# Performance work log

Hardware: AMD Instinct MI355X
Metric: run time of the kernel (lower is better)

Reference implementation:

```python
import jax, jax.numpy as jnp
import numpy as np

B, C, H, W = 4, 64, 128, 128
KS = 3
PAD = 1
N = KS * KS


def conv2d(x, w, b=None, stride=1, padding=0):
    out = jax.lax.conv_general_dilated(
        x, w, (stride, stride), [(padding, padding), (padding, padding)],
        dimension_numbers=("NCHW", "OIHW", "NCHW"))
    if b is not None:
        out = out + b[None, :, None, None]
    return out


def setup_inputs() -> dict:
    key = jax.random.key(0)
    ks = jax.random.split(key, 6)
    scale = 0.05  # small weights so offsets stay in a realistic range
    return {
        "x": jax.random.normal(ks[0], (B, C, H, W), jnp.float32),
        "p_w": jax.random.normal(ks[1], (2 * N, C, 3, 3), jnp.float32) * scale,
        "p_b": jax.random.normal(ks[2], (2 * N,), jnp.float32) * scale,
        "m_w": jax.random.normal(ks[3], (N, C, 3, 3), jnp.float32) * scale,
        "m_b": jax.random.normal(ks[4], (N,), jnp.float32) * scale,
        "conv_w": jax.random.normal(ks[5], (C, C, KS, KS), jnp.float32) * (1.0 / np.sqrt(C * N)),
    }


def reference(x, p_w, p_b, m_w, m_b, conv_w):
    b, c, h, w = x.shape
    # offset / modulation branches (stride=1, padding=1, 3x3)
    offset = conv2d(x, p_w, p_b, 1, 1)                 # (b, 2N, h, w)
    m = jax.nn.sigmoid(conv2d(x, m_w, m_b, 1, 1))      # (b, N,  h, w)

    xp = jnp.pad(x, ((0, 0), (0, 0), (PAD, PAD), (PAD, PAD)))
    Hp, Wp = h + 2 * PAD, w + 2 * PAD

    # sampling positions p = p_0 + p_n + offset, layout (b, h, w, 2N): first N rows(x), last N cols(y)
    pnx, pny = jnp.meshgrid(jnp.arange(-1, 2), jnp.arange(-1, 2), indexing="ij")
    p_n = jnp.concatenate([pnx.ravel(), pny.ravel()]).astype(x.dtype)          # (2N,)
    base_x = jnp.broadcast_to(jnp.arange(1, h + 1)[:, None, None], (h, w, N))
    base_y = jnp.broadcast_to(jnp.arange(1, w + 1)[None, :, None], (h, w, N))
    base = jnp.concatenate([base_x, base_y], axis=-1).astype(x.dtype)          # (h, w, 2N)
    p = jnp.transpose(offset, (0, 2, 3, 1)) + p_n + base[None]                 # (b, h, w, 2N)

    px, py = p[..., :N], p[..., N:]
    # integer corners from detached p (floor), clamped to padded extent
    qf = jnp.floor(jax.lax.stop_gradient(p))
    qx_lt = jnp.clip(qf[..., :N], 0, Hp - 1).astype(jnp.int32)
    qy_lt = jnp.clip(qf[..., N:], 0, Wp - 1).astype(jnp.int32)
    qx_rb = jnp.clip(qf[..., :N] + 1, 0, Hp - 1).astype(jnp.int32)
    qy_rb = jnp.clip(qf[..., N:] + 1, 0, Wp - 1).astype(jnp.int32)

    pxc = jnp.clip(px, 0, Hp - 1)
    pyc = jnp.clip(py, 0, Wp - 1)

    g_lt = (1 + (qx_lt - pxc)) * (1 + (qy_lt - pyc))
    g_rb = (1 - (qx_rb - pxc)) * (1 - (qy_rb - pyc))
    g_lb = (1 + (qx_lt - pxc)) * (1 - (qy_rb - pyc))
    g_rt = (1 - (qx_rb - pxc)) * (1 + (qy_lt - pyc))

    xp_flat = xp.reshape(b, c, Hp * Wp)

    def gather(qx, qy):
        idx = (qx * Wp + qy).reshape(b, -1)                     # (b, h*w*N)
        out = jax.vmap(lambda xf, i: xf[:, i])(xp_flat, idx)    # (b, c, h*w*N)
        return out.reshape(b, c, h, w, N)

    x_off = (g_lt[:, None] * gather(qx_lt, qy_lt)
             + g_rb[:, None] * gather(qx_rb, qy_rb)
             + g_lb[:, None] * gather(qx_lt, qy_rb)
             + g_rt[:, None] * gather(qx_rb, qy_lt))            # (b, c, h, w, N)

    x_off = x_off * jnp.transpose(m, (0, 2, 3, 1))[:, None]     # modulation

    # _reshape_x_offset: n = 3*i + j -> (b, c, h*3, w*3) with layout (h, i, w, j)
    x_off = x_off.reshape(b, c, h, w, KS, KS)
    x_off = jnp.transpose(x_off, (0, 1, 2, 4, 3, 5)).reshape(b, c, h * KS, w * KS)

    return conv2d(x_off, conv_w, None, stride=KS, padding=0)    # (b, outc, h, w)
```

## Files before the change

### kernel.cpp

```cpp
#include <hip/hip_runtime.h>
#include <hip/hip_bf16.h>
#include <math.h>

#define BB 4
#define CC 64
#define HH 128
#define WW 128
#define NPT 9
#define HW (HH*WW)
#define HP 130
#define WP 130

typedef __attribute__((ext_vector_type(8))) short bf16x8;
typedef __attribute__((ext_vector_type(4))) float f32x4;

static __device__ __forceinline__ unsigned short f2bf(float f) {
    __hip_bfloat16 h = __float2bfloat16(f);
    return *reinterpret_cast<unsigned short*>(&h);
}
static __device__ __forceinline__ float bf2f(unsigned short u) {
    return __uint_as_float(((unsigned int)u) << 16);
}

__global__ void k_prep(const float* __restrict__ cw,
                       const float* __restrict__ pw, const float* __restrict__ pb,
                       const float* __restrict__ mw, const float* __restrict__ mb,
                       unsigned short* __restrict__ wtt, unsigned short* __restrict__ wttB,
                       float* __restrict__ b27, unsigned short* __restrict__ xt) {
    int i = blockIdx.x * 256 + threadIdx.x;
    if (i < 36864) {
        int cot = i / 9216;
        int rem = i - cot * 9216;
        int n   = rem >> 10;
        int s2  = (rem >> 9) & 1;
        int lhi = (rem >> 7) & 3;
        int l15 = (rem >> 3) & 15;
        int j   = i & 7;
        int co = cot * 16 + l15;
        int ci = s2 * 32 + lhi * 8 + j;
        wtt[i] = f2bf(cw[(co * 64 + ci) * 9 + n]);
    } else if (i < 55296) {
        int q = i - 36864;
        int j   = q & 7;
        int co  = (q >> 3) & 31;
        int lhi = (q >> 8) & 3;
        int s2  = (q >> 10) & 1;
        int n   = q >> 11;
        int ci  = s2 * 32 + lhi * 8 + j;
        float v = 0.f;
        if (co < 18) v = pw[(co * 64 + ci) * 9 + n];
        else if (co < 27) v = mw[((co - 18) * 64 + ci) * 9 + n];
        wttB[q] = f2bf(v);
    } else if (i < 55328) {
        int co = i - 55296;
        b27[co] = (co < 18) ? pb[co] : (co < 27 ? mb[co - 18] : 0.f);
    } else if (i < 55328 + BB * 4128) {
        int p = i - 55328;
        int b = p / 4128, r = p - b * 4128;
        size_t base;
        if (r < 2080) {
            int row = r / 1040;
            int rr  = r - row * 1040;
            int wp = rr >> 3, c8 = rr & 7;
            int hp = row ? (HP - 1) : 0;
            base = (((size_t)b * HP + hp) * WP + wp) * 64 + c8 * 8;
        } else {
            int r2 = r - 2080;
            int col = r2 >> 10;
            int rr  = r2 & 1023;
            int hp = (rr >> 3) + 1, c8 = rr & 7;
            int wp = col ? (WP - 1) : 0;
            base = (((size_t)b * HP + hp) * WP + wp) * 64 + c8 * 8;
        }
        *reinterpret_cast<int4*>(xt + base) = make_int4(0, 0, 0, 0);
    }
}

__global__ __launch_bounds__(256) void k_nhwc(const float* __restrict__ x,
                                              unsigned short* __restrict__ xt) {
    __shared__ float tile[64][129];
    int blk = blockIdx.x;
    int b = blk >> 7, h = blk & 127;
    int t = threadIdx.x;
    const float* xb = x + ((size_t)b * CC) * HW + h * WW;
    #pragma unroll
    for (int i = 0; i < 32; ++i) {
        int idx = i * 256 + t;
        int ci = idx >> 7, w = idx & 127;
        tile[ci][w] = xb[(size_t)ci * HW + w];
    }
    __syncthreads();
    unsigned short* xtb = xt + (((size_t)b * HP + (h + 1)) * WP + 1) * 64;
    #pragma unroll
    for (int i = 0; i < 32; ++i) {
        int idx = i * 256 + t;
        int w = idx >> 6, ci = idx & 63;
        xtb[(size_t)w * 64 + ci] = f2bf(tile[ci][w]);
    }
}

#define OMS 68
#define NCX 198

union SmemU {
    struct { int geo[576 * 8]; unsigned int xoff[2048]; } d;
    unsigned short astage[NCX * 64];
};

__global__ __launch_bounds__(512, 4) void k_fused(
    const unsigned short* __restrict__ xt, const unsigned short* __restrict__ wttB,
    const float* __restrict__ b27, const unsigned short* __restrict__ wtt,
    float* __restrict__ out)
{
    __shared__ SmemU su;
    __shared__ float s_om[27 * OMS];

    int blk0 = blockIdx.x;
    int blk = (blk0 & 7) * 128 + (blk0 >> 3);
    int wblk = blk & 1;
    int h = (blk >> 1) & 127;
    int b = blk >> 8;
    int w0 = wblk * 64;
    int t = threadIdx.x;
    int ln = t & 63, wid = t >> 6;
    int ln15 = ln & 15, lhi = ln >> 4;

    const unsigned short* xtb = xt + (size_t)b * HP * WP * 64;
    char* astage_c = reinterpret_cast<char*>(su.astage);

    for (int uu = t; uu < NCX * 8; uu += 512) {
        int cx = uu >> 3, o16 = uu & 7;
        int r = cx / 66, c = cx - r * 66;
        const unsigned short* src = xtb + ((size_t)(h + r) * WP + (w0 + c)) * 64 + o16 * 8;
        int4 v = *reinterpret_cast<const int4*>(src);
        *reinterpret_cast<int4*>(astage_c + cx * 128 + ((o16 ^ (cx & 7)) << 4)) = v;
    }
    __syncthreads();

    {
        int pxg = wid >> 1, coh = wid & 1;
        int px = pxg * 16 + ln15;
        f32x4 acc;
        acc[0] = 0.f; acc[1] = 0.f; acc[2] = 0.f; acc[3] = 0.f;
        const unsigned short* wB = wttB + (size_t)(coh * 16 + ln15) * 8 + lhi * 256;
        bf16x8 bfc = *reinterpret_cast<const bf16x8*>(wB);
        #pragma unroll
        for (int ns = 0; ns < 18; ++ns) {
            bf16x8 bfn = bfc;
            if (ns < 17)
                bfn = *reinterpret_cast<const bf16x8*>(wB + (size_t)(ns + 1) * 1024);
            int n = ns >> 1, s2 = ns & 1;
            int kh = n / 3, kw = n - kh * 3;
            int cx = kh * 66 + px + kw;
            int o16 = s2 * 4 + lhi;
            bf16x8 af = *reinterpret_cast<const bf16x8*>(
                astage_c + cx * 128 + ((o16 ^ (cx & 7)) << 4));
            acc = __builtin_amdgcn_mfma_f32_16x16x32_bf16(af, bfc, acc, 0, 0, 0);
            bfc = bfn;
        }
        int co = coh * 16 + ln15;
        int prow = pxg * 16 + lhi * 4;
        if (co < 27) {
            float bias = b27[co];
            float4 v;
            v.x = acc[0] + bias; v.y = acc[1] + bias;
            v.z = acc[2] + bias; v.w = acc[3] + bias;
            if (co >= 18) {
                v.x = 1.f / (1.f + expf(-v.x));
                v.y = 1.f / (1.f + expf(-v.y));
                v.z = 1.f / (1.f + expf(-v.z));
                v.w = 1.f / (1.f + expf(-v.w));
            }
            *reinterpret_cast<float4*>(&s_om[co * OMS + prow]) = v;
        }
    }
    __syncthreads();

    int* s_geo = su.d.geo;

    for (int idx = t; idx < NPT * 64; idx += 512) {
        int n = idx >> 6, px = idx & 63;
        float ox = s_om[n * OMS + px];
        float oy = s_om[(9 + n) * OMS + px];
        float mk = s_om[(18 + n) * OMS + px];
        float pxf = ox + (float)(n / 3 - 1) + (float)(h + 1);
        float pyf = oy + (float)(n % 3 - 1) + (float)(w0 + px + 1);
        float fx = floorf(pxf), fy = floorf(pyf);
        int qxlt = (int)fminf(fmaxf(fx, 0.f), 129.f);
        int qylt = (int)fminf(fmaxf(fy, 0.f), 129.f);
        int qxrb = (int)fminf(fmaxf(fx + 1.f, 0.f), 129.f);
        int qyrb = (int)fminf(fmaxf(fy + 1.f, 0.f), 129.f);
        float pxc = fminf(fmaxf(pxf, 0.f), 129.f);
        float pyc = fminf(fmaxf(pyf, 0.f), 129.f);
        float ax = 1.f + (float)qxlt - pxc;
        float bx = 1.f - ((float)qxrb - pxc);
        float ay = 1.f + (float)qylt - pyc;
        float by = 1.f - ((float)qyrb - pyc);
        int* g = &s_geo[idx * 8];
        g[0] = (qxlt * WP + qylt) * 64;
        g[1] = (qxrb * WP + qyrb) * 64;
        g[2] = (qxlt * WP + qyrb) * 64;
        g[3] = (qxrb * WP + qylt) * 64;
        reinterpret_cast<float*>(g)[4] = ax * ay * mk;
        reinterpret_cast<float*>(g)[5] = bx * by * mk;
        reinterpret_cast<float*>(g)[6] = ax * by * mk;
        reinterpret_cast<float*>(g)[7] = bx * ay * mk;
    }
    __syncthreads();

    f32x4 acc[2];
    #pragma unroll
    for (int g = 0; g < 2; ++g) {
        acc[g][0] = 0.f; acc[g][1] = 0.f; acc[g][2] = 0.f; acc[g][3] = 0.f;
    }

    const unsigned short* wbase = wtt + (size_t)(wid & 3) * 9216;
    int px_s = t >> 3;
    int cig_s = t & 7;
    int coff = cig_s * 8;
    char* xoff_base = reinterpret_cast<char*>(su.d.xoff);
    int ghalf = wid >> 2;

    bf16x8 c0, c1, c2, c3;
    {
        const int* gp = &s_geo[px_s * 8];
        int a0 = gp[0], a1 = gp[1], a2 = gp[2], a3 = gp[3];
        c0 = *reinterpret_cast<const bf16x8*>(xtb + a0 + coff);
        c1 = *reinterpret_cast<const bf16x8*>(xtb + a1 + coff);
        c2 = *reinterpret_cast<const bf16x8*>(xtb + a2 + coff);
        c3 = *reinterpret_cast<const bf16x8*>(xtb + a3 + coff);
    }

    for (int n = 0; n < NPT; ++n) {
        bf16x8 d0 = c0, d1 = c1, d2 = c2, d3 = c3;
        if (n < NPT - 1) {
            const int* gpn = &s_geo[((n + 1) * 64 + px_s) * 8];
            int na0 = gpn[0], na1 = gpn[1], na2 = gpn[2], na3 = gpn[3];
            d0 = *reinterpret_cast<const bf16x8*>(xtb + na0 + coff);
            d1 = *reinterpret_cast<const bf16x8*>(xtb + na1 + coff);
            d2 = *reinterpret_cast<const bf16x8*>(xtb + na2 + coff);
            d3 = *reinterpret_cast<const bf16x8*>(xtb + na3 + coff);
        }
        bf16x8 bf0 = *reinterpret_cast<const bf16x8*>(wbase + n * 1024 + lhi * 128 + ln15 * 8);
        bf16x8 bf1 = *reinterpret_cast<const bf16x8*>(wbase + n * 1024 + 512 + lhi * 128 + ln15 * 8);

        const float* wp = reinterpret_cast<const float*>(&s_geo[(n * 64 + px_s) * 8]) + 4;
        float glt = wp[0], grb = wp[1], glb = wp[2], grt = wp[3];

        unsigned int pk[4];
        #pragma unroll
        for (int i = 0; i < 4; ++i) {
            float va = glt * bf2f((unsigned short)c0[2*i])   + grb * bf2f((unsigned short)c1[2*i])
                     + glb * bf2f((unsigned short)c2[2*i])   + grt * bf2f((unsigned short)c3[2*i]);
            float vb = glt * bf2f((unsigned short)c0[2*i+1]) + grb * bf2f((unsigned short)c1[2*i+1])
                     + glb * bf2f((unsigned short)c2[2*i+1]) + grt * bf2f((unsigned short)c3[2*i+1]);
            pk[i] = (unsigned int)f2bf(va) | ((unsigned int)f2bf(vb) << 16);
        }
        {
            char* base = xoff_base + px_s * 128;
            int sw = (px_s & 7) << 4;
            *reinterpret_cast<int4*>(base + ((cig_s * 16) ^ sw)) = *reinterpret_cast<int4*>(&pk[0]);
        }
        __syncthreads();

        #pragma unroll
        for (int s2 = 0; s2 < 2; ++s2) {
            bf16x8 bfr = s2 ? bf1 : bf0;
            #pragma unroll
            for (int g = 0; g < 2; ++g) {
                int row = (ghalf * 2 + g) * 16 + ln15;
                int cb2 = (s2 * 32 + lhi * 8) * 2;
                bf16x8 af = *reinterpret_cast<const bf16x8*>(
                    xoff_base + row * 128 + (cb2 ^ ((row & 7) << 4)));
                acc[g] = __builtin_amdgcn_mfma_f32_16x16x32_bf16(af, bfr, acc[g], 0, 0, 0);
            }
        }
        __syncthreads();

        c0 = d0; c1 = d1; c2 = d2; c3 = d3;
    }

    int co = (wid & 3) * 16 + ln15;
    float* orow = out + ((size_t)b * CC + co) * HW + h * WW + w0;
    #pragma unroll
    for (int g = 0; g < 2; ++g) {
        *reinterpret_cast<float4*>(orow + (ghalf * 2 + g) * 16 + lhi * 4) =
            *reinterpret_cast<float4*>(&acc[g]);
    }
}

extern "C" void kernel_launch(void* const* d_in, const int* in_sizes, int n_in,
                              void* d_out, int out_size, void* d_ws, size_t ws_size,
                              hipStream_t stream) {
    const float* x  = (const float*)d_in[0];
    const float* pw = (const float*)d_in[1];
    const float* pb = (const float*)d_in[2];
    const float* mw = (const float*)d_in[3];
    const float* mb = (const float*)d_in[4];
    const float* cw = (const float*)d_in[5];
    float* out = (float*)d_out;

    char* wsc = (char*)d_ws;
    unsigned short* xt  = (unsigned short*)wsc;
    size_t off = ((size_t)BB * HP * WP * 64 * 2 + 255) & ~(size_t)255;
    unsigned short* wtt = (unsigned short*)(wsc + off);
    off += (size_t)64 * 576 * 2;
    unsigned short* wttB = (unsigned short*)(wsc + off);
    off += (size_t)18432 * 2;
    float* b27 = (float*)(wsc + ((off + 255) & ~(size_t)255));

    int prep_items = 36864 + 18432 + 32 + BB * 4128;
    hipLaunchKernelGGL(k_prep, dim3((prep_items + 255) / 256), dim3(256), 0, stream,
                       cw, pw, pb, mw, mb, wtt, wttB, b27, xt);
    hipLaunchKernelGGL(k_nhwc, dim3(BB * HH), dim3(256), 0, stream, x, xt);
    hipLaunchKernelGGL(k_fused, dim3(BB * HH * 2), dim3(512), 0, stream,
                       xt, wttB, b27, wtt, out);
}
```

Baseline: 45.50 us.

## Double-buffer sampled tile in LDS and merge prep kernels into one launch

The per-tap loop in the fused kernel now uses two LDS buffers for the bilinear-sampled activations. Gathers run two taps ahead and the next tap is packed while MFMAs consume the current one, so one barrier per tap replaces two. The NHWC transpose kernel and the weight-prep kernel are merged into a single launch to save one kernel launch. The extra LDS buffer and extra live gather registers may lower occupancy.

```diff
diff --git a/kernel.cpp b/kernel.cpp
--- a/kernel.cpp
+++ b/kernel.cpp
@@ -22,12 +22,36 @@
     return __uint_as_float(((unsigned int)u) << 16);
 }
 
-__global__ void k_prep(const float* __restrict__ cw,
-                       const float* __restrict__ pw, const float* __restrict__ pb,
-                       const float* __restrict__ mw, const float* __restrict__ mb,
-                       unsigned short* __restrict__ wtt, unsigned short* __restrict__ wttB,
-                       float* __restrict__ b27, unsigned short* __restrict__ xt) {
-    int i = blockIdx.x * 256 + threadIdx.x;
+__global__ __launch_bounds__(256) void k_pre(
+    const float* __restrict__ x, const float* __restrict__ cw,
+    const float* __restrict__ pw, const float* __restrict__ pb,
+    const float* __restrict__ mw, const float* __restrict__ mb,
+    unsigned short* __restrict__ xt, unsigned short* __restrict__ wtt,
+    unsigned short* __restrict__ wttB, float* __restrict__ b27)
+{
+    __shared__ float tile[64][129];
+    int bid = blockIdx.x;
+    int t = threadIdx.x;
+    if (bid < BB * HH) {
+        int b = bid >> 7, h = bid & 127;
+        const float* xb = x + ((size_t)b * CC) * HW + h * WW;
+        #pragma unroll
+        for (int i = 0; i < 32; ++i) {
+            int idx = i * 256 + t;
+            int ci = idx >> 7, w = idx & 127;
+            tile[ci][w] = xb[(size_t)ci * HW + w];
+        }
+        __syncthreads();
+        unsigned short* xtb = xt + (((size_t)b * HP + (h + 1)) * WP + 1) * 64;
+        #pragma unroll
+        for (int i = 0; i < 32; ++i) {
+            int idx = i * 256 + t;
+            int w = idx >> 6, ci = idx & 63;
+            xtb[(size_t)w * 64 + ci] = f2bf(tile[ci][w]);
+        }
+        return;
+    }
+    int i = (bid - BB * HH) * 256 + t;
     if (i < 36864) {
         int cot = i / 9216;
         int rem = i - cot * 9216;
@@ -76,34 +100,11 @@
     }
 }
 
-__global__ __launch_bounds__(256) void k_nhwc(const float* __restrict__ x,
-                                              unsigned short* __restrict__ xt) {
-    __shared__ float tile[64][129];
-    int blk = blockIdx.x;
-    int b = blk >> 7, h = blk & 127;
-    int t = threadIdx.x;
-    const float* xb = x + ((size_t)b * CC) * HW + h * WW;
-    #pragma unroll
-    for (int i = 0; i < 32; ++i) {
-        int idx = i * 256 + t;
-        int ci = idx >> 7, w = idx & 127;
-        tile[ci][w] = xb[(size_t)ci * HW + w];
-    }
-    __syncthreads();
-    unsigned short* xtb = xt + (((size_t)b * HP + (h + 1)) * WP + 1) * 64;
-    #pragma unroll
-    for (int i = 0; i < 32; ++i) {
-        int idx = i * 256 + t;
-        int w = idx >> 6, ci = idx & 63;
-        xtb[(size_t)w * 64 + ci] = f2bf(tile[ci][w]);
-    }
-}
-
 #define OMS 68
 #define NCX 198
 
 union SmemU {
-    struct { int geo[576 * 8]; unsigned int xoff[2048]; } d;
+    struct { int geo[576 * 8]; unsigned int xoff[2][2048]; } d;
     unsigned short astage[NCX * 64];
 };
 
@@ -220,65 +221,83 @@
     int coff = cig_s * 8;
     char* xoff_base = reinterpret_cast<char*>(su.d.xoff);
     int ghalf = wid >> 2;
-
-    bf16x8 c0, c1, c2, c3;
-    {
-        const int* gp = &s_geo[px_s * 8];
-        int a0 = gp[0], a1 = gp[1], a2 = gp[2], a3 = gp[3];
-        c0 = *reinterpret_cast<const bf16x8*>(xtb + a0 + coff);
-        c1 = *reinterpret_cast<const bf16x8*>(xtb + a1 + coff);
-        c2 = *reinterpret_cast<const bf16x8*>(xtb + a2 + coff);
-        c3 = *reinterpret_cast<const bf16x8*>(xtb + a3 + coff);
-    }
-
-    for (int n = 0; n < NPT; ++n) {
-        bf16x8 d0 = c0, d1 = c1, d2 = c2, d3 = c3;
-        if (n < NPT - 1) {
-            const int* gpn = &s_geo[((n + 1) * 64 + px_s) * 8];
-            int na0 = gpn[0], na1 = gpn[1], na2 = gpn[2], na3 = gpn[3];
-            d0 = *reinterpret_cast<const bf16x8*>(xtb + na0 + coff);
-            d1 = *reinterpret_cast<const bf16x8*>(xtb + na1 + coff);
-            d2 = *reinterpret_cast<const bf16x8*>(xtb + na2 + coff);
-            d3 = *reinterpret_cast<const bf16x8*>(xtb + na3 + coff);
-        }
-        bf16x8 bf0 = *reinterpret_cast<const bf16x8*>(wbase + n * 1024 + lhi * 128 + ln15 * 8);
-        bf16x8 bf1 = *reinterpret_cast<const bf16x8*>(wbase + n * 1024 + 512 + lhi * 128 + ln15 * 8);
-
-        const float* wp = reinterpret_cast<const float*>(&s_geo[(n * 64 + px_s) * 8]) + 4;
-        float glt = wp[0], grb = wp[1], glb = wp[2], grt = wp[3];
-
-        unsigned int pk[4];
-        #pragma unroll
-        for (int i = 0; i < 4; ++i) {
-            float va = glt * bf2f((unsigned short)c0[2*i])   + grb * bf2f((unsigned short)c1[2*i])
-                     + glb * bf2f((unsigned short)c2[2*i])   + grt * bf2f((unsigned short)c3[2*i]);
-            float vb = glt * bf2f((unsigned short)c0[2*i+1]) + grb * bf2f((unsigned short)c1[2*i+1])
-                     + glb * bf2f((unsigned short)c2[2*i+1]) + grt * bf2f((unsigned short)c3[2*i+1]);
-            pk[i] = (unsigned int)f2bf(va) | ((unsigned int)f2bf(vb) << 16);
-        }
-        {
-            char* base = xoff_base + px_s * 128;
-            int sw = (px_s & 7) << 4;
-            *reinterpret_cast<int4*>(base + ((cig_s * 16) ^ sw)) = *reinterpret_cast<int4*>(&pk[0]);
-        }
-        __syncthreads();
-
-        #pragma unroll
-        for (int s2 = 0; s2 < 2; ++s2) {
-            bf16x8 bfr = s2 ? bf1 : bf0;
-            #pragma unroll
-            for (int g = 0; g < 2; ++g) {
-                int row = (ghalf * 2 + g) * 16 + ln15;
-                int cb2 = (s2 * 32 + lhi * 8) * 2;
-                bf16x8 af = *reinterpret_cast<const bf16x8*>(
-                    xoff_base + row * 128 + (cb2 ^ ((row & 7) << 4)));
-                acc[g] = __builtin_amdgcn_mfma_f32_16x16x32_bf16(af, bfr, acc[g], 0, 0, 0);
-            }
-        }
-        __syncthreads();
-
-        c0 = d0; c1 = d1; c2 = d2; c3 = d3;
-    }
+    int wsw = (cig_s * 16) ^ ((px_s & 7) << 4);
+
+    bf16x8 ga0, ga1, ga2, ga3, gb0, gb1, gb2, gb3;
+
+#define GATHER(S0, S1, S2, S3, NN) do {                                        \
+        const int* gp_ = &s_geo[((NN) * 64 + px_s) * 8];                       \
+        S0 = *reinterpret_cast<const bf16x8*>(xtb + gp_[0] + coff);            \
+        S1 = *reinterpret_cast<const bf16x8*>(xtb + gp_[1] + coff);            \
+        S2 = *reinterpret_cast<const bf16x8*>(xtb + gp_[2] + coff);            \
+        S3 = *reinterpret_cast<const bf16x8*>(xtb + gp_[3] + coff);            \
+    } while (0)
+
+#define PACK(S0, S1, S2, S3, NN) do {                                          \
+        const float* wp_ = reinterpret_cast<const float*>(                     \
+            &s_geo[((NN) * 64 + px_s) * 8]) + 4;                               \
+        float glt_ = wp_[0], grb_ = wp_[1], glb_ = wp_[2], grt_ = wp_[3];      \
+        unsigned int pk_[4];                                                   \
+        _Pragma("unroll")                                                      \
+        for (int i_ = 0; i_ < 4; ++i_) {                                       \
+            float va_ = glt_ * bf2f((unsigned short)S0[2*i_])                  \
+                      + grb_ * bf2f((unsigned short)S1[2*i_])                  \
+                      + glb_ * bf2f((unsigned short)S2[2*i_])                  \
+                      + grt_ * bf2f((unsigned short)S3[2*i_]);                 \
+            float vb_ = glt_ * bf2f((unsigned short)S0[2*i_+1])                \
+                      + grb_ * bf2f((unsigned short)S1[2*i_+1])                \
+                      + glb_ * bf2f((unsigned short)S2[2*i_+1])                \
+                      + grt_ * bf2f((unsigned short)S3[2*i_+1]);               \
+            pk_[i_] = (unsigned int)f2bf(va_) | ((unsigned int)f2bf(vb_) << 16); \
+        }                                                                      \
+        *reinterpret_cast<int4*>(xoff_base + ((NN) & 1) * 8192 + px_s * 128 + wsw) \
+            = *reinterpret_cast<int4*>(&pk_[0]);                               \
+    } while (0)
+
+#define MFMA_N(NN) do {                                                        \
+        bf16x8 bf0_ = *reinterpret_cast<const bf16x8*>(                        \
+            wbase + (NN) * 1024 + lhi * 128 + ln15 * 8);                       \
+        bf16x8 bf1_ = *reinterpret_cast<const bf16x8*>(                        \
+            wbase + (NN) * 1024 + 512 + lhi * 128 + ln15 * 8);                 \
+        char* rbuf_ = xoff_base + ((NN) & 1) * 8192;                           \
+        _Pragma("unroll")                                                      \
+        for (int s2_ = 0; s2_ < 2; ++s2_) {                                    \
+            bf16x8 bfr_ = s2_ ? bf1_ : bf0_;                                   \
+            _Pragma("unroll")                                                  \
+            for (int g_ = 0; g_ < 2; ++g_) {                                   \
+                int row_ = (ghalf * 2 + g_) * 16 + ln15;                       \
+                int cb2_ = (s2_ * 32 + lhi * 8) * 2;                           \
+                bf16x8 af_ = *reinterpret_cast<const bf16x8*>(                 \
+                    rbuf_ + row_ * 128 + (cb2_ ^ ((row_ & 7) << 4)));          \
+                acc[g_] = __builtin_amdgcn_mfma_f32_16x16x32_bf16(             \
+                    af_, bfr_, acc[g_], 0, 0, 0);                              \
+            }                                                                  \
+        }                                                                      \
+    } while (0)
+
+    GATHER(ga0, ga1, ga2, ga3, 0);
+    GATHER(gb0, gb1, gb2, gb3, 1);
+    PACK(ga0, ga1, ga2, ga3, 0);
+    __syncthreads();
+
+#define DSTEP(NN, N0, N1, N2, N3, P0, P1, P2, P3) do {                         \
+        if ((NN) + 2 < NPT) GATHER(N0, N1, N2, N3, (NN) + 2);                  \
+        MFMA_N(NN);                                                            \
+        if ((NN) + 1 < NPT) {                                                  \
+            PACK(P0, P1, P2, P3, (NN) + 1);                                    \
+            __syncthreads();                                                   \
+        }                                                                      \
+    } while (0)
+
+    DSTEP(0, ga0, ga1, ga2, ga3, gb0, gb1, gb2, gb3);
+    DSTEP(1, gb0, gb1, gb2, gb3, ga0, ga1, ga2, ga3);
+    DSTEP(2, ga0, ga1, ga2, ga3, gb0, gb1, gb2, gb3);
+    DSTEP(3, gb0, gb1, gb2, gb3, ga0, ga1, ga2, ga3);
+    DSTEP(4, ga0, ga1, ga2, ga3, gb0, gb1, gb2, gb3);
+    DSTEP(5, gb0, gb1, gb2, gb3, ga0, ga1, ga2, ga3);
+    DSTEP(6, ga0, ga1, ga2, ga3, gb0, gb1, gb2, gb3);
+    DSTEP(7, gb0, gb1, gb2, gb3, ga0, ga1, ga2, ga3);
+    DSTEP(8, ga0, ga1, ga2, ga3, gb0, gb1, gb2, gb3);
 
     int co = (wid & 3) * 16 + ln15;
     float* orow = out + ((size_t)b * CC + co) * HW + h * WW + w0;
@@ -310,9 +329,9 @@
     float* b27 = (float*)(wsc + ((off + 255) & ~(size_t)255));
 
     int prep_items = 36864 + 18432 + 32 + BB * 4128;
-    hipLaunchKernelGGL(k_prep, dim3((prep_items + 255) / 256), dim3(256), 0, stream,
-                       cw, pw, pb, mw, mb, wtt, wttB, b27, xt);
-    hipLaunchKernelGGL(k_nhwc, dim3(BB * HH), dim3(256), 0, stream, x, xt);
+    int prep_blocks = (prep_items + 255) / 256;
+    hipLaunchKernelGGL(k_pre, dim3(BB * HH + prep_blocks), dim3(256), 0, stream,
+                       x, cw, pw, pb, mw, mb, xt, wtt, wttB, b27);
     hipLaunchKernelGGL(k_fused, dim3(BB * HH * 2), dim3(512), 0, stream,
                        xt, wttB, b27, wtt, out);
 }
```

Result: faster. 40.94 us (-10.0%).
